# Optimization experiments

Measured on AMD Instinct MI355X. Metric: run time of the kernel, lower is better.

## Reference

```python
import jax, jax.numpy as jnp
import numpy as np

B = 4194304  # number of sequential rows


def setup_inputs() -> dict:
    key = jax.random.key(0)
    k1, k2, k3, k4 = jax.random.split(key, 4)
    x = jax.random.normal(k1, (B, 1, 3), dtype=jnp.float32)
    # nn.Linear(3, 3) params
    lim = 1.0 / np.sqrt(3.0)
    W = jax.random.uniform(k2, (3, 3), minval=-lim, maxval=lim, dtype=jnp.float32)
    b = jax.random.uniform(k3, (3,), minval=-lim, maxval=lim, dtype=jnp.float32)
    # FastNetwork init: (-1-1)*rand([3,1]) + 1  -> uniform in [-1, 1]
    net0 = jax.random.uniform(k4, (3, 1), minval=-1.0, maxval=1.0, dtype=jnp.float32)
    return {"x": x, "W": W, "b": b, "net0": net0}


def reference(x, W, b, net0):
    # x: [B,1,3]; W: [3,3]; b: [3]; net0: [3,1]
    xi = x[:, 0, :]                      # [B,3]
    # Updater: per-row Linear(3,3) -- batched as one matmul
    updates = xi @ W.T + b               # [B,3]

    def step(net, inp):
        x_row, u = inp                   # x_row: [3], u: [3]
        # 1/(1+exp(-10*(net + update - 0.5))) == sigmoid(10*(net + update - 0.5))
        net = jax.nn.sigmoid(10.0 * (net + u[:, None] - 0.5))  # [3,1]
        pred = x_row @ net               # [1]
        return net, pred

    _, preds = jax.lax.scan(step, net0, (xi, updates))
    return preds                         # [B,1]
```

## Files before the change

### kernel.cpp

```cpp
#include <hip/hip_runtime.h>


#if __has_builtin(__builtin_amdgcn_exp2f)
#define EXP2F(v) __builtin_amdgcn_exp2f(v)
#else
#define EXP2F(v) __expf(0.6931471805599453f * (v))
#endif

namespace {
constexpr int   BTOT   = 4194304;
constexpr int   CHUNK  = 32;
constexpr int   BLOCK  = 256;
constexpr int   BSTEPS = BLOCK * CHUNK;
constexpr int   WARM   = 64;
constexpr int   GRID   = BTOT / BSTEPS;
constexpr float KEXP   = -14.426950408889634f;
constexpr float EPS    = 1e-5f;
}

#define CVALS(X0_, X1_, X2_)                                                   \
  const float c0 = fmaf(kw00, (X0_), fmaf(kw01, (X1_), fmaf(kw02, (X2_), kb0))); \
  const float c1 = fmaf(kw10, (X0_), fmaf(kw11, (X1_), fmaf(kw12, (X2_), kb1))); \
  const float c2 = fmaf(kw20, (X0_), fmaf(kw21, (X1_), fmaf(kw22, (X2_), kb2)));

#define SIG(N, C) __builtin_amdgcn_rcpf(1.0f + EXP2F(fmaf(KEXP, (N), (C))))

#define PULL(VAL_, AD_) \
  __int_as_float(__builtin_amdgcn_ds_bpermute((AD_), __float_as_int(VAL_)))

#define FETCH1(S_, XD0, XD1, XD2)                                              \
  if ((S_) < 32) {                                                             \
    XD0 = PULL(fx[3 * (S_) + 0], a2);                                          \
    XD1 = PULL(fx[3 * (S_) + 1], a2);                                          \
    XD2 = PULL(fx[3 * (S_) + 2], a2);                                          \
    if (lane < 2) {                                                            \
      const float4 wv_ = wb[(S_) + (lane << 5)];                               \
      XD0 = wv_.x; XD1 = wv_.y; XD2 = wv_.z;                                   \
    }                                                                          \
  } else {                                                                     \
    XD0 = PULL(fx[3 * ((S_) - 32) + 0], a1);                                   \
    XD1 = PULL(fx[3 * ((S_) - 32) + 1], a1);                                   \
    XD2 = PULL(fx[3 * ((S_) - 32) + 2], a1);                                   \
    if (lane < 1) {                                                            \
      const float4 wv_ = wb[(S_)];                                             \
      XD0 = wv_.x; XD1 = wv_.y; XD2 = wv_.z;                                   \
    }                                                                          \
  }

#define DSTEP(X0_, X1_, X2_)                                                   \
  {                                                                            \
    CVALS(X0_, X1_, X2_)                                                       \
    lo0 = SIG(lo0, c0); hi0 = SIG(hi0, c0);                                    \
    lo1 = SIG(lo1, c1); hi1 = SIG(hi1, c1);                                    \
    lo2 = SIG(lo2, c2); hi2 = SIG(hi2, c2);                                    \
  }

#define SSTEP(X0_, X1_, X2_)                                                   \
  {                                                                            \
    CVALS(X0_, X1_, X2_)                                                       \
    m0 = SIG(m0, c0); m1 = SIG(m1, c1); m2 = SIG(m2, c2);                      \
  }

#define WBATCH(B_)                                                             \
  {                                                                            \
    float X00,X01,X02,X10,X11,X12,X20,X21,X22,X30,X31,X32;                     \
    FETCH1(4*(B_)+0, X00, X01, X02)                                            \
    FETCH1(4*(B_)+1, X10, X11, X12)                                            \
    FETCH1(4*(B_)+2, X20, X21, X22)                                            \
    FETCH1(4*(B_)+3, X30, X31, X32)                                            \
    if (!single) {                                                             \
      DSTEP(X00, X01, X02) DSTEP(X10, X11, X12)                                \
      DSTEP(X20, X21, X22) DSTEP(X30, X31, X32)                                \
      conv = ((hi0 - lo0) < EPS) & ((hi1 - lo1) < EPS) & ((hi2 - lo2) < EPS);  \
      if (__all(conv)) {                                                       \
        m0 = 0.5f * (lo0 + hi0); m1 = 0.5f * (lo1 + hi1);                      \
        m2 = 0.5f * (lo2 + hi2);                                               \
        single = true;                                                         \
      }                                                                        \
    } else {                                                                   \
      SSTEP(X00, X01, X02) SSTEP(X10, X11, X12)                                \
      SSTEP(X20, X21, X22) SSTEP(X30, X31, X32)                                \
    }                                                                          \
  }

#define MS(P_, X0_, X1_, X2_)                                                  \
  {                                                                            \
    CVALS(X0_, X1_, X2_)                                                       \
    m0 = SIG(m0, c0); m1 = SIG(m1, c1); m2 = SIG(m2, c2);                      \
    P_ = fmaf((X0_), m0, fmaf((X1_), m1, (X2_) * m2));                         \
  }

__global__ __launch_bounds__(BLOCK, 2) void Updater_65395172049297_kernel(
    const float* __restrict__ x, const float* __restrict__ W,
    const float* __restrict__ bv, const float* __restrict__ n0v,
    float* __restrict__ out)
{
    __shared__ float4 wbuf[BLOCK / 64][WARM];

    const float kw00 = KEXP * W[0], kw01 = KEXP * W[1], kw02 = KEXP * W[2];
    const float kw10 = KEXP * W[3], kw11 = KEXP * W[4], kw12 = KEXP * W[5];
    const float kw20 = KEXP * W[6], kw21 = KEXP * W[7], kw22 = KEXP * W[8];
    const float kb0 = KEXP * (bv[0] - 0.5f);
    const float kb1 = KEXP * (bv[1] - 0.5f);
    const float kb2 = KEXP * (bv[2] - 0.5f);
    const float n00 = n0v[0], n01 = n0v[1], n02 = n0v[2];

    const int  lane  = threadIdx.x & 63;
    const int  w     = threadIdx.x >> 6;
    const long S     = (long)blockIdx.x * BSTEPS;
    const long start = S + (long)threadIdx.x * CHUNK;
    const int  a1    = ((lane >= 1) ? (lane - 1) : 0) << 2;
    const int  a2    = ((lane >= 2) ? (lane - 2) : 0) << 2;
    const float4* wb = wbuf[w];

    float4 wv;
    {
        const long wbase = S + (long)w * (64 * CHUNK);
        long sstep = wbase - WARM + lane;
        if (sstep < 0) sstep = 0;
        const float* xp = x + 3 * sstep;
        wv = make_float4(xp[0], xp[1], xp[2], 0.0f);
    }

    float fx[96];
    {
        const float4* mp = reinterpret_cast<const float4*>(x + 3 * start);
#pragma unroll
        for (int i = 0; i < 24; ++i) {
            const float4 v = mp[i];
            fx[4 * i + 0] = v.x; fx[4 * i + 1] = v.y;
            fx[4 * i + 2] = v.z; fx[4 * i + 3] = v.w;
        }
    }

    wbuf[w][lane] = wv;

    const bool exact   = (start <= (long)WARM);
    const int  smin    = exact ? (int)(WARM - (int)start) : 0;
    const bool special = (blockIdx.x == 0) && (w == 0);

    float lo0, lo1, lo2, hi0, hi1, hi2;
    if (exact) { lo0 = hi0 = n00; lo1 = hi1 = n01; lo2 = hi2 = n02; }
    else       { lo0 = lo1 = lo2 = 0.0f; hi0 = hi1 = hi2 = 1.0f; }

    bool  conv = false, single = false;
    float m0 = n00, m1 = n01, m2 = n02;

    if (special) {
        for (int s = 0; s < WARM; ++s) {
            if (s >= smin) {
                const long as_ = start - WARM + s;
                const float X0 = x[3 * as_], X1 = x[3 * as_ + 1], X2 = x[3 * as_ + 2];
                DSTEP(X0, X1, X2)
            }
        }
        conv = ((hi0 - lo0) < EPS) & ((hi1 - lo1) < EPS) & ((hi2 - lo2) < EPS);
        if (__all(conv)) {
            m0 = 0.5f * (lo0 + hi0); m1 = 0.5f * (lo1 + hi1); m2 = 0.5f * (lo2 + hi2);
            single = true;
        }
    } else {
        WBATCH(0)  WBATCH(1)  WBATCH(2)  WBATCH(3)
        WBATCH(4)  WBATCH(5)  WBATCH(6)  WBATCH(7)
        WBATCH(8)  WBATCH(9)  WBATCH(10) WBATCH(11)
        WBATCH(12) WBATCH(13) WBATCH(14) WBATCH(15)
    }

    if (!single) {
        for (int at = 1; at < 10 && !conv; ++at) {
            long wl2 = (long)WARM << (2 * at);
            long bgn = start - wl2;
            bool ex2 = (bgn <= 0);
            if (ex2) bgn = 0;
            if (ex2) { lo0 = hi0 = n00; lo1 = hi1 = n01; lo2 = hi2 = n02; }
            else     { lo0 = lo1 = lo2 = 0.0f; hi0 = hi1 = hi2 = 1.0f; }
            const float4* bp = reinterpret_cast<const float4*>(x + 3 * bgn);
            const long ng = (start - bgn) >> 2;
            for (long q = 0; q < ng; ++q) {
                const float4 A4 = bp[3 * q], B4 = bp[3 * q + 1], C4 = bp[3 * q + 2];
                DSTEP(A4.x, A4.y, A4.z)
                DSTEP(A4.w, B4.x, B4.y)
                DSTEP(B4.z, B4.w, C4.x)
                DSTEP(C4.y, C4.z, C4.w)
            }
            conv = ex2 || (((hi0 - lo0) < EPS) & ((hi1 - lo1) < EPS) &
                           ((hi2 - lo2) < EPS));
        }
        m0 = 0.5f * (lo0 + hi0); m1 = 0.5f * (lo1 + hi1); m2 = 0.5f * (lo2 + hi2);
    }

    float4* op = reinterpret_cast<float4*>(out + start);
#pragma unroll
    for (int q = 0; q < 8; ++q) {
        float p0, p1, p2, p3;
        MS(p0, fx[12 * q + 0], fx[12 * q + 1],  fx[12 * q + 2]);
        MS(p1, fx[12 * q + 3], fx[12 * q + 4],  fx[12 * q + 5]);
        MS(p2, fx[12 * q + 6], fx[12 * q + 7],  fx[12 * q + 8]);
        MS(p3, fx[12 * q + 9], fx[12 * q + 10], fx[12 * q + 11]);
        op[q] = make_float4(p0, p1, p2, p3);
    }
}

extern "C" void kernel_launch(void* const* d_in, const int* in_sizes, int n_in,
                              void* d_out, int out_size, void* d_ws, size_t ws_size,
                              hipStream_t stream) {
    const float* x   = (const float*)d_in[0];
    const float* W   = (const float*)d_in[1];
    const float* bv  = (const float*)d_in[2];
    const float* n0v = (const float*)d_in[3];
    float*       out = (float*)d_out;
    Updater_65395172049297_kernel<<<GRID, BLOCK, 0, stream>>>(x, W, bv, n0v, out);
}
```

Baseline: 106.4 us.

## Halve per-thread chunk and warmup, stage input loads through LDS for coalescing

```diff
diff --git a/kernel.cpp b/kernel.cpp
--- a/kernel.cpp
+++ b/kernel.cpp
@@ -9,11 +9,12 @@
 
 namespace {
 constexpr int   BTOT   = 4194304;
-constexpr int   CHUNK  = 32;
+constexpr int   CHUNK  = 16;
 constexpr int   BLOCK  = 256;
 constexpr int   BSTEPS = BLOCK * CHUNK;
-constexpr int   WARM   = 64;
+constexpr int   WARM   = 32;
 constexpr int   GRID   = BTOT / BSTEPS;
+constexpr int   QW     = 52;
 constexpr float KEXP   = -14.426950408889634f;
 constexpr float EPS    = 1e-5f;
 }
@@ -29,18 +30,18 @@
   __int_as_float(__builtin_amdgcn_ds_bpermute((AD_), __float_as_int(VAL_)))
 
 #define FETCH1(S_, XD0, XD1, XD2)                                              \
-  if ((S_) < 32) {                                                             \
-    XD0 = PULL(fx[3 * (S_) + 0], a2);                                          \
-    XD1 = PULL(fx[3 * (S_) + 1], a2);                                          \
-    XD2 = PULL(fx[3 * (S_) + 2], a2);                                          \
+  if ((S_) < 16) {                                                             \
+    XD0 = PULL(fx[3 * (S_) + 0], pa2);                                         \
+    XD1 = PULL(fx[3 * (S_) + 1], pa2);                                         \
+    XD2 = PULL(fx[3 * (S_) + 2], pa2);                                         \
     if (lane < 2) {                                                            \
-      const float4 wv_ = wb[(S_) + (lane << 5)];                               \
+      const float4 wv_ = wb[(S_) + (lane << 4)];                               \
       XD0 = wv_.x; XD1 = wv_.y; XD2 = wv_.z;                                   \
     }                                                                          \
   } else {                                                                     \
-    XD0 = PULL(fx[3 * ((S_) - 32) + 0], a1);                                   \
-    XD1 = PULL(fx[3 * ((S_) - 32) + 1], a1);                                   \
-    XD2 = PULL(fx[3 * ((S_) - 32) + 2], a1);                                   \
+    XD0 = PULL(fx[3 * ((S_) - 16) + 0], pa1);                                  \
+    XD1 = PULL(fx[3 * ((S_) - 16) + 1], pa1);                                  \
+    XD2 = PULL(fx[3 * ((S_) - 16) + 2], pa1);                                  \
     if (lane < 1) {                                                            \
       const float4 wv_ = wb[(S_)];                                             \
       XD0 = wv_.x; XD1 = wv_.y; XD2 = wv_.z;                                   \
@@ -90,11 +91,21 @@
     P_ = fmaf((X0_), m0, fmaf((X1_), m1, (X2_) * m2));                         \
   }
 
-__global__ __launch_bounds__(BLOCK, 2) void Updater_65395172049297_kernel(
+#define STW(P_, O_, V_) *reinterpret_cast<float4*>((P_) + (O_)) = (V_);
+#define RDQ(P_)                                                                \
+  _Pragma("unroll")                                                            \
+  for (int j = 0; j < 12; ++j) {                                               \
+    const float4 v = *reinterpret_cast<const float4*>((P_) + rb + 4 * j);      \
+    fx[4 * j + 0] = v.x; fx[4 * j + 1] = v.y;                                  \
+    fx[4 * j + 2] = v.z; fx[4 * j + 3] = v.w;                                  \
+  }
+
+__global__ __launch_bounds__(BLOCK, 4) void Updater_65395172049297_kernel(
     const float* __restrict__ x, const float* __restrict__ W,
     const float* __restrict__ bv, const float* __restrict__ n0v,
     float* __restrict__ out)
 {
+    __shared__ float  qbuf[BLOCK / 64][2][16 * QW];
     __shared__ float4 wbuf[BLOCK / 64][WARM];
 
     const float kw00 = KEXP * W[0], kw01 = KEXP * W[1], kw02 = KEXP * W[2];
@@ -108,32 +119,48 @@
     const int  lane  = threadIdx.x & 63;
     const int  w     = threadIdx.x >> 6;
     const long S     = (long)blockIdx.x * BSTEPS;
-    const long start = S + (long)threadIdx.x * CHUNK;
-    const int  a1    = ((lane >= 1) ? (lane - 1) : 0) << 2;
-    const int  a2    = ((lane >= 2) ? (lane - 2) : 0) << 2;
+    const long Wb    = S + (long)w * (64 * CHUNK);
+    const long start = Wb + (long)lane * CHUNK;
+    const int  pa1   = ((lane >= 1) ? (lane - 1) : 0) << 2;
+    const int  pa2   = ((lane >= 2) ? (lane - 2) : 0) << 2;
     const float4* wb = wbuf[w];
 
     float4 wv;
-    {
-        const long wbase = S + (long)w * (64 * CHUNK);
-        long sstep = wbase - WARM + lane;
+    if (lane < WARM) {
+        long sstep = Wb - WARM + lane;
         if (sstep < 0) sstep = 0;
         const float* xp = x + 3 * sstep;
         wv = make_float4(xp[0], xp[1], xp[2], 0.0f);
     }
 
-    float fx[96];
+    const float4* xw = reinterpret_cast<const float4*>(x) +
+                       ((long)blockIdx.x * 3072 + (long)w * 768);
+    const int g0  = lane, g1 = 64 + lane, g2 = 128 + lane;
+    const int wa0 = (g0 / 12) * QW + (g0 % 12) * 4;
+    const int wa1 = (g1 / 12) * QW + (g1 % 12) * 4;
+    const int wa2 = (g2 / 12) * QW + (g2 % 12) * 4;
+    float* A  = qbuf[w][0];
+    float* Bf = qbuf[w][1];
+    const int myq = lane >> 4;
+    const int rb  = (lane & 15) * QW;
+
+    float fx[48];
     {
-        const float4* mp = reinterpret_cast<const float4*>(x + 3 * start);
-#pragma unroll
-        for (int i = 0; i < 24; ++i) {
-            const float4 v = mp[i];
-            fx[4 * i + 0] = v.x; fx[4 * i + 1] = v.y;
-            fx[4 * i + 2] = v.z; fx[4 * i + 3] = v.w;
-        }
-    }
-
-    wbuf[w][lane] = wv;
+        float4 r0 = xw[g0],       r1 = xw[g1],       r2 = xw[g2];
+        float4 s0 = xw[192 + g0], s1 = xw[192 + g1], s2 = xw[192 + g2];
+        STW(A, wa0, r0) STW(A, wa1, r1) STW(A, wa2, r2)
+        if (myq == 0) { RDQ(A) }
+        r0 = xw[384 + g0]; r1 = xw[384 + g1]; r2 = xw[384 + g2];
+        STW(Bf, wa0, s0) STW(Bf, wa1, s1) STW(Bf, wa2, s2)
+        if (myq == 1) { RDQ(Bf) }
+        s0 = xw[576 + g0]; s1 = xw[576 + g1]; s2 = xw[576 + g2];
+        STW(A, wa0, r0) STW(A, wa1, r1) STW(A, wa2, r2)
+        if (myq == 2) { RDQ(A) }
+        STW(Bf, wa0, s0) STW(Bf, wa1, s1) STW(Bf, wa2, s2)
+        if (myq == 3) { RDQ(Bf) }
+    }
+
+    if (lane < WARM) wbuf[w][lane] = wv;
 
     const bool exact   = (start <= (long)WARM);
     const int  smin    = exact ? (int)(WARM - (int)start) : 0;
@@ -160,10 +187,8 @@
             single = true;
         }
     } else {
-        WBATCH(0)  WBATCH(1)  WBATCH(2)  WBATCH(3)
-        WBATCH(4)  WBATCH(5)  WBATCH(6)  WBATCH(7)
-        WBATCH(8)  WBATCH(9)  WBATCH(10) WBATCH(11)
-        WBATCH(12) WBATCH(13) WBATCH(14) WBATCH(15)
+        WBATCH(0) WBATCH(1) WBATCH(2) WBATCH(3)
+        WBATCH(4) WBATCH(5) WBATCH(6) WBATCH(7)
     }
 
     if (!single) {
@@ -191,7 +216,7 @@
 
     float4* op = reinterpret_cast<float4*>(out + start);
 #pragma unroll
-    for (int q = 0; q < 8; ++q) {
+    for (int q = 0; q < 4; ++q) {
         float p0, p1, p2, p3;
         MS(p0, fx[12 * q + 0], fx[12 * q + 1],  fx[12 * q + 2]);
         MS(p1, fx[12 * q + 3], fx[12 * q + 4],  fx[12 * q + 5]);
```

Measured after the change: 127.3 us. +19.7%, slower.
